# Kernel tuning notes

Measured on AMD Instinct MI355X. Metric: run time of the kernel, lower is better.

Reference implementation:

```python
import jax, jax.numpy as jnp
import numpy as np

B, T, C, H, E, K = 4, 2048, 1024, 2048, 8, 2


def setup_inputs() -> dict:
    key = jax.random.key(0)
    ks = jax.random.split(key, 9)
    s = lambda k, shape, fan: jax.random.normal(k, shape, jnp.float32) / np.sqrt(fan)
    return {
        "x": jax.random.normal(ks[0], (B, T, C), jnp.float32),
        "gate_w": s(ks[1], (C, E), C),            # router gate (no bias)
        "sg_w": s(ks[2], (C, H), C),              # shared expert: gate proj
        "su_w": s(ks[3], (C, H), C),              # shared expert: up proj
        "sd_w": s(ks[4], (H, C), H),              # shared expert: down proj
        "eg_w": s(ks[5], (E, C, H), C),           # routed experts: gate proj
        "eu_w": s(ks[6], (E, C, H), C),           # routed experts: up proj
        "ed_w": s(ks[7], (E, H, C), H),           # routed experts: down proj
    }


def _swiglu(x, wg, wu, wd):
    # x: (B,T,C) -> (B,T,C)
    return jnp.einsum("bth,hc->btc", jax.nn.silu(jnp.einsum("btc,ch->bth", x, wg)) * jnp.einsum("btc,ch->bth", x, wu), wd)


def reference(x, gate_w, sg_w, su_w, sd_w, eg_w, eu_w, ed_w):
    # Router: top-k over expert logits, softmax over selected logits
    logits = jnp.einsum("btc,ce->bte", x, gate_w)            # (B,T,E)
    topk_logits, topk_idx = jax.lax.top_k(logits, K)         # (B,T,K)
    weights = jax.nn.softmax(topk_logits, axis=-1)           # (B,T,K)
    # Dense per-expert combine weight: w_e[b,t,e] = sum_k weights*(idx==e)
    onehot = jax.nn.one_hot(topk_idx, E, dtype=x.dtype)      # (B,T,K,E)
    dense_w = jnp.einsum("btk,btke->bte", weights, onehot)   # (B,T,E)

    shared_out = _swiglu(x, sg_w, su_w, sd_w)

    # Scan over experts (small fixed E), accumulating weighted expert outputs.
    dense_w_e = jnp.moveaxis(dense_w, -1, 0)                 # (E,B,T)

    def step(acc, params):
        wg, wu, wd, w = params
        return acc + w[..., None] * _swiglu(x, wg, wu, wd), None

    expert_out, _ = jax.lax.scan(step, jnp.zeros_like(x), (eg_w, eu_w, ed_w, dense_w_e))
    return shared_out + expert_out, logits
```

## Files before the change

### kernel.cpp

```cpp
#include <hip/hip_runtime.h>
#include <cstdint>
#include <cstddef>

#define NTOK 8192
#define CDIM 1024
#define HDIM 2048
#define NEXP 8
#define NSEG 9
#define MAXTILES 104

typedef __bf16 bf16;
typedef unsigned short u16;
typedef __attribute__((ext_vector_type(8))) __bf16 bf16x8;
typedef __attribute__((ext_vector_type(4))) float f32x4;

__device__ __forceinline__ u16 f2bf(float f) {
  union { u16 u; __bf16 b; } cv;
  cv.b = (__bf16)f;
  return cv.u;
}

__device__ __forceinline__ void gload_lds16(const bf16* g, bf16* l) {
  __builtin_amdgcn_global_load_lds(
      (const __attribute__((address_space(1))) unsigned int*)g,
      (__attribute__((address_space(3))) unsigned int*)l, 16, 0, 0);
}

__global__ __launch_bounds__(64) void init_kernel(int* __restrict__ counts,
                                                  int* __restrict__ fill) {
  if (threadIdx.x < NEXP) {
    counts[threadIdx.x] = 0;
    fill[threadIdx.x] = 0;
  }
}

__global__ __launch_bounds__(256) void zero_out_kernel(float* __restrict__ out) {
  size_t i = ((size_t)blockIdx.x * 256 + threadIdx.x) * 8;
  float4 z = {0.f, 0.f, 0.f, 0.f};
  *(float4*)(out + i) = z;
  *(float4*)(out + i + 4) = z;
}

__global__ __launch_bounds__(256) void cast_x_kernel(
    const float* __restrict__ src, bf16* __restrict__ dst) {
  size_t i = ((size_t)blockIdx.x * 256 + threadIdx.x) * 8;
  float4 a = *(const float4*)(src + i);
  float4 b = *(const float4*)(src + i + 4);
  bf16x8 p;
  p[0] = (bf16)a.x; p[1] = (bf16)a.y; p[2] = (bf16)a.z; p[3] = (bf16)a.w;
  p[4] = (bf16)b.x; p[5] = (bf16)b.y; p[6] = (bf16)b.z; p[7] = (bf16)b.w;
  *(bf16x8*)(dst + i) = p;
}

__global__ __launch_bounds__(256) void router2_kernel(
    const float* __restrict__ x, const float* __restrict__ gw,
    float* __restrict__ logits_out, int* __restrict__ tk_e,
    float* __restrict__ tk_w, int* __restrict__ counts) {
  int wv = threadIdx.x >> 6, l = threadIdx.x & 63;
  int t = blockIdx.x * 4 + wv;
  const float* xr = x + (size_t)t * CDIM;
  float acc[NEXP];
#pragma unroll
  for (int e = 0; e < NEXP; ++e) acc[e] = 0.f;
  for (int c = l; c < CDIM; c += 64) {
    float xv = xr[c];
    const float* g = gw + (size_t)c * NEXP;
    float4 g0 = *(const float4*)(g);
    float4 g1 = *(const float4*)(g + 4);
    acc[0] += xv * g0.x; acc[1] += xv * g0.y; acc[2] += xv * g0.z; acc[3] += xv * g0.w;
    acc[4] += xv * g1.x; acc[5] += xv * g1.y; acc[6] += xv * g1.z; acc[7] += xv * g1.w;
  }
#pragma unroll
  for (int off = 32; off > 0; off >>= 1) {
#pragma unroll
    for (int e = 0; e < NEXP; ++e) acc[e] += __shfl_xor(acc[e], off, 64);
  }
  int e0 = 0; float l0 = acc[0];
#pragma unroll
  for (int e = 1; e < NEXP; ++e) { if (acc[e] > l0) { l0 = acc[e]; e0 = e; } }
  int e1 = -1; float l1 = -3.4e38f;
#pragma unroll
  for (int e = 0; e < NEXP; ++e) { if (e != e0 && acc[e] > l1) { l1 = acc[e]; e1 = e; } }
  float ex = expf(l1 - l0);
  float w0 = 1.f / (1.f + ex), w1 = ex / (1.f + ex);
  if (l < NEXP) logits_out[(size_t)t * NEXP + l] = acc[l];
  if (l == 0) {
    tk_e[2 * t] = e0; tk_e[2 * t + 1] = e1;
    tk_w[2 * t] = w0; tk_w[2 * t + 1] = w1;
    atomicAdd(&counts[e0], 1);
    atomicAdd(&counts[e1], 1);
  }
}

__global__ __launch_bounds__(256) void offsets_kernel(
    const int* __restrict__ counts, int* __restrict__ offs_g,
    int* __restrict__ tile_seg, int* __restrict__ list_tok,
    float* __restrict__ w_row) {
  __shared__ int off[NSEG], pad[NSEG], cnt[NSEG], ntot;
  int tid = threadIdx.x;
  if (tid == 0) {
    int tot = 0;
    for (int e = 0; e < NSEG; ++e) {
      int c = (e < NEXP) ? counts[e] : NTOK;
      cnt[e] = c; off[e] = tot;
      int p = (c + 255) & ~255;
      pad[e] = p; tot += p;
    }
    ntot = tot;
  }
  __syncthreads();
  if (tid < NSEG) offs_g[tid] = off[tid];
  for (int gt = tid; gt < MAXTILES; gt += 256) {
    int row = gt * 256, seg = -1;
    if (row < ntot) {
      for (int e = 0; e < NSEG; ++e)
        if (row >= off[e] && row < off[e] + pad[e]) { seg = e; break; }
    }
    tile_seg[gt] = seg;
  }
  for (int e = 0; e < NSEG; ++e)
    for (int i = off[e] + cnt[e] + tid; i < off[e] + pad[e]; i += 256) {
      list_tok[i] = 0;
      w_row[i] = 0.f;
    }
}

__global__ __launch_bounds__(256) void scatter_kernel(
    const int* __restrict__ tk_e, const float* __restrict__ tk_w,
    const int* __restrict__ offs, int* __restrict__ fill,
    int* __restrict__ list_tok, float* __restrict__ w_row) {
  int t = blockIdx.x * 256 + threadIdx.x;
  int e0 = tk_e[2 * t], e1 = tk_e[2 * t + 1];
  float w0 = tk_w[2 * t], w1 = tk_w[2 * t + 1];
  int p0 = atomicAdd(&fill[e0], 1);
  int i0 = offs[e0] + p0;
  list_tok[i0] = t; w_row[i0] = w0;
  int p1 = atomicAdd(&fill[e1], 1);
  int i1 = offs[e1] + p1;
  list_tok[i1] = t; w_row[i1] = w1;
  int rsh = offs[NEXP] + t;
  list_tok[rsh] = t; w_row[rsh] = 1.f;
}

__device__ __forceinline__ void transpose_body(const float* __restrict__ src,
                                               u16* __restrict__ dst, int R, int C) {
  __shared__ u16 tile[64][65];
  int r0 = blockIdx.y * 64, c0 = blockIdx.x * 64;
  int tr = threadIdx.x >> 2;
  int tc = (threadIdx.x & 3) * 16;
  const float* s = src + (size_t)(r0 + tr) * C + c0 + tc;
  float4 f[4];
#pragma unroll
  for (int q = 0; q < 4; ++q) f[q] = *(const float4*)(s + q * 4);
#pragma unroll
  for (int q = 0; q < 4; ++q) {
    tile[tr][tc + q * 4 + 0] = f2bf(f[q].x);
    tile[tr][tc + q * 4 + 1] = f2bf(f[q].y);
    tile[tr][tc + q * 4 + 2] = f2bf(f[q].z);
    tile[tr][tc + q * 4 + 3] = f2bf(f[q].w);
  }
  __syncthreads();
  union { uint4 v[2]; u16 e[16]; } u;
#pragma unroll
  for (int j = 0; j < 16; ++j) u.e[j] = tile[tc + j][tr];
  u16* d = dst + (size_t)(c0 + tr) * R + r0 + tc;
  *(uint4*)d = u.v[0];
  *(uint4*)(d + 8) = u.v[1];
}

__global__ __launch_bounds__(256) void transpose_cast_kernel(
    const float* __restrict__ src, u16* __restrict__ dst, int R, int C) {
  transpose_body(src, dst, R, C);
}

__global__ __launch_bounds__(256) void transpose_gu_kernel(
    const float* __restrict__ sg, const float* __restrict__ su,
    const float* __restrict__ eg, const float* __restrict__ eu,
    u16* __restrict__ wTg, u16* __restrict__ wTu) {
  const size_t slot = (size_t)HDIM * CDIM;
  int z = blockIdx.z;
  const float* src; u16* dst;
  if (z == 0)       { src = sg;                 dst = wTg + 8 * slot; }
  else if (z == 1)  { src = su;                 dst = wTu + 8 * slot; }
  else if (z < 10)  { src = eg + (z - 2) * slot;  dst = wTg + (z - 2) * slot; }
  else              { src = eu + (z - 10) * slot; dst = wTu + (z - 10) * slot; }
  transpose_body(src, dst, CDIM, HDIM);
}

__global__ __launch_bounds__(256) void transpose_d_kernel(
    const float* __restrict__ sd, const float* __restrict__ ed,
    u16* __restrict__ wTd) {
  const size_t slot = (size_t)HDIM * CDIM;
  int z = blockIdx.z;
  const float* src; u16* dst;
  if (z == 0) { src = sd;                 dst = wTd + 8 * slot; }
  else        { src = ed + (z - 1) * slot; dst = wTd + (z - 1) * slot; }
  transpose_body(src, dst, HDIM, CDIM);
}


__global__ __launch_bounds__(512, 2) void gemm_gu2(
    const bf16* __restrict__ xb, const bf16* __restrict__ wTg,
    const bf16* __restrict__ wTu, const int* __restrict__ tile_seg,
    const int* __restrict__ list_tok, bf16* __restrict__ act) {
  __shared__ __align__(16) bf16 sA[2][256 * 64];
  __shared__ __align__(16) bf16 sBg[2][128 * 64];
  __shared__ __align__(16) bf16 sBu[2][128 * 64];
  __shared__ int tokLds[256];

  const int nwg = gridDim.x;
  const int bid = blockIdx.x;
  const int wid = (bid & 7) * (nwg >> 3) + (bid >> 3);
  const int tileIdx = wid % MAXTILES;
  const int colIdx = wid / MAXTILES;
  const int seg = tile_seg[tileIdx];
  if (seg < 0) return;

  const int tid = threadIdx.x, l = tid & 63, wv = tid >> 6;
  const int wr = wv >> 1, wc = wv & 1;
  const int n0 = colIdx * 128;
  const size_t rowbase = (size_t)tileIdx * 256;

  if (tid < 256) tokLds[tid] = list_tok[rowbase + tid];
  __syncthreads();

  const int srow = tid >> 3;
  const int scolSw = ((tid & 7) ^ (srow & 7)) << 3;
  const bf16* baseA[4];
#pragma unroll
  for (int q = 0; q < 4; ++q)
    baseA[q] = xb + (size_t)tokLds[q * 64 + srow] * CDIM + scolSw;
  const size_t wslot = (size_t)seg * HDIM * CDIM;
  const bf16* baseBg[2];
  const bf16* baseBu[2];
#pragma unroll
  for (int q = 0; q < 2; ++q) {
    const size_t r = (size_t)(n0 + q * 64 + srow) * CDIM + scolSw;
    baseBg[q] = wTg + wslot + r;
    baseBu[q] = wTu + wslot + r;
  }
  const int ldst = tid * 8;

  const int fr = l & 15;
  const int aRowB = (wr * 64 + fr) * 128;
  const int bRowB = (wc * 64 + fr) * 128;
  const int cSw0 = (((l >> 4) ^ (l & 7)) << 4);
  const int cSw1 = (((4 | (l >> 4)) ^ (l & 7)) << 4);

  f32x4 accG[4][4], accU[4][4];
#pragma unroll
  for (int i = 0; i < 4; ++i)
#pragma unroll
    for (int j = 0; j < 4; ++j) {
      accG[i][j] = (f32x4){0.f, 0.f, 0.f, 0.f};
      accU[i][j] = (f32x4){0.f, 0.f, 0.f, 0.f};
    }

  auto stage = [&](int b, int k0) {
#pragma unroll
    for (int q = 0; q < 4; ++q)
      gload_lds16(baseA[q] + k0, &sA[b][q * 4096 + ldst]);
#pragma unroll
    for (int q = 0; q < 2; ++q) {
      gload_lds16(baseBg[q] + k0, &sBg[b][q * 4096 + ldst]);
      gload_lds16(baseBu[q] + k0, &sBu[b][q * 4096 + ldst]);
    }
  };
  auto compute = [&](int b) {
    const char* pA = (const char*)&sA[b][0];
    const char* pG = (const char*)&sBg[b][0];
    const char* pU = (const char*)&sBu[b][0];
#pragma unroll
    for (int kk = 0; kk < 2; ++kk) {
      const int cSw = kk ? cSw1 : cSw0;
      bf16x8 af[4], bg[4], bu[4];
#pragma unroll
      for (int i = 0; i < 4; ++i) af[i] = *(const bf16x8*)(pA + aRowB + i * 2048 + cSw);
#pragma unroll
      for (int j = 0; j < 4; ++j) bg[j] = *(const bf16x8*)(pG + bRowB + j * 2048 + cSw);
#pragma unroll
      for (int j = 0; j < 4; ++j) bu[j] = *(const bf16x8*)(pU + bRowB + j * 2048 + cSw);
#pragma unroll
      for (int i = 0; i < 4; ++i)
#pragma unroll
        for (int j = 0; j < 4; ++j) {
          accG[i][j] = __builtin_amdgcn_mfma_f32_16x16x32_bf16(af[i], bg[j], accG[i][j], 0, 0, 0);
          accU[i][j] = __builtin_amdgcn_mfma_f32_16x16x32_bf16(af[i], bu[j], accU[i][j], 0, 0, 0);
        }
    }
  };

  const int NKT = CDIM / 64;
  stage(0, 0);
  for (int kt = 0; kt < NKT; kt += 2) {
    __syncthreads();
    stage(1, (kt + 1) * 64);
    compute(0);
    __syncthreads();
    if (kt + 2 < NKT) stage(0, (kt + 2) * 64);
    compute(1);
  }

  const int cn = n0 + wc * 64 + fr;
  const int rb = wr * 64 + (l >> 4) * 4;
#pragma unroll
  for (int i = 0; i < 4; ++i)
#pragma unroll
    for (int r = 0; r < 4; ++r) {
      const size_t row = rowbase + rb + i * 16 + r;
#pragma unroll
      for (int j = 0; j < 4; ++j) {
        float g = accG[i][j][r], u = accU[i][j][r];
        float s = g / (1.f + expf(-g));
        act[row * HDIM + cn + j * 16] = (bf16)(s * u);
      }
    }
}

__global__ __launch_bounds__(512, 2) void gemm_down2(
    const bf16* __restrict__ act, const bf16* __restrict__ wTd,
    const int* __restrict__ tile_seg, const int* __restrict__ list_tok,
    const float* __restrict__ w_row, float* __restrict__ out) {
  __shared__ __align__(16) bf16 sA[2][256 * 64];
  __shared__ __align__(16) bf16 sB[2][128 * 64];
  __shared__ int tokLds[256];
  __shared__ float wLds[256];

  const int nwg = gridDim.x;
  const int bid = blockIdx.x;
  const int wid = (bid & 7) * (nwg >> 3) + (bid >> 3);
  const int tileIdx = wid % MAXTILES;
  const int colIdx = wid / MAXTILES;
  const int seg = tile_seg[tileIdx];
  if (seg < 0) return;

  const int tid = threadIdx.x, l = tid & 63, wv = tid >> 6;
  const int wr = wv >> 1, wc = wv & 1;
  const int n0 = colIdx * 128;
  const size_t rowbase = (size_t)tileIdx * 256;

  if (tid < 256) tokLds[tid] = list_tok[rowbase + tid];
  else           wLds[tid - 256] = w_row[rowbase + tid - 256];
  __syncthreads();

  const int srow = tid >> 3;
  const int scolSw = ((tid & 7) ^ (srow & 7)) << 3;
  const bf16* baseA[4];
#pragma unroll
  for (int q = 0; q < 4; ++q)
    baseA[q] = act + (rowbase + q * 64 + srow) * HDIM + scolSw;
  const bf16* baseB[2];
#pragma unroll
  for (int q = 0; q < 2; ++q)
    baseB[q] = wTd + (size_t)seg * CDIM * HDIM + (size_t)(n0 + q * 64 + srow) * HDIM + scolSw;
  const int ldst = tid * 8;

  const int fr = l & 15;
  const int aRowB = (wr * 64 + fr) * 128;
  const int bRowB = (wc * 64 + fr) * 128;
  const int cSw0 = (((l >> 4) ^ (l & 7)) << 4);
  const int cSw1 = (((4 | (l >> 4)) ^ (l & 7)) << 4);

  f32x4 acc[4][4];
#pragma unroll
  for (int i = 0; i < 4; ++i)
#pragma unroll
    for (int j = 0; j < 4; ++j) acc[i][j] = (f32x4){0.f, 0.f, 0.f, 0.f};

  auto stage = [&](int b, int k0) {
#pragma unroll
    for (int q = 0; q < 4; ++q)
      gload_lds16(baseA[q] + k0, &sA[b][q * 4096 + ldst]);
#pragma unroll
    for (int q = 0; q < 2; ++q)
      gload_lds16(baseB[q] + k0, &sB[b][q * 4096 + ldst]);
  };
  auto compute = [&](int b) {
    const char* pA = (const char*)&sA[b][0];
    const char* pB = (const char*)&sB[b][0];
#pragma unroll
    for (int kk = 0; kk < 2; ++kk) {
      const int cSw = kk ? cSw1 : cSw0;
      bf16x8 af[4], bfr[4];
#pragma unroll
      for (int i = 0; i < 4; ++i) af[i] = *(const bf16x8*)(pA + aRowB + i * 2048 + cSw);
#pragma unroll
      for (int j = 0; j < 4; ++j) bfr[j] = *(const bf16x8*)(pB + bRowB + j * 2048 + cSw);
#pragma unroll
      for (int i = 0; i < 4; ++i)
#pragma unroll
        for (int j = 0; j < 4; ++j)
          acc[i][j] = __builtin_amdgcn_mfma_f32_16x16x32_bf16(af[i], bfr[j], acc[i][j], 0, 0, 0);
    }
  };

  const int NKT = HDIM / 64;
  stage(0, 0);
  for (int kt = 0; kt < NKT; kt += 2) {
    __syncthreads();
    stage(1, (kt + 1) * 64);
    compute(0);
    __syncthreads();
    if (kt + 2 < NKT) stage(0, (kt + 2) * 64);
    compute(1);
  }

  const int cn = n0 + wc * 64 + fr;
  const int rb = wr * 64 + (l >> 4) * 4;
#pragma unroll
  for (int i = 0; i < 4; ++i)
#pragma unroll
    for (int r = 0; r < 4; ++r) {
      const int lrow = rb + i * 16 + r;
      const float w = wLds[lrow];
      if (w != 0.f) {
        const int tok = tokLds[lrow];
        float* op = out + (size_t)tok * CDIM + cn;
#pragma unroll
        for (int j = 0; j < 4; ++j)
          atomicAdd(op + j * 16, w * acc[i][j][r]);
      }
    }
}

__global__ __launch_bounds__(256) void router_kernel(
    const float* __restrict__ x, const float* __restrict__ gw,
    float* __restrict__ dense_w, float* __restrict__ logits_out) {
  int wv = threadIdx.x >> 6, l = threadIdx.x & 63;
  int t = blockIdx.x * 4 + wv;
  const float* xr = x + (size_t)t * CDIM;
  float acc[NEXP];
#pragma unroll
  for (int e = 0; e < NEXP; ++e) acc[e] = 0.f;
  for (int c = l; c < CDIM; c += 64) {
    float xv = xr[c];
    const float* g = gw + (size_t)c * NEXP;
    float4 g0 = *(const float4*)(g);
    float4 g1 = *(const float4*)(g + 4);
    acc[0] += xv * g0.x; acc[1] += xv * g0.y; acc[2] += xv * g0.z; acc[3] += xv * g0.w;
    acc[4] += xv * g1.x; acc[5] += xv * g1.y; acc[6] += xv * g1.z; acc[7] += xv * g1.w;
  }
#pragma unroll
  for (int off = 32; off > 0; off >>= 1) {
#pragma unroll
    for (int e = 0; e < NEXP; ++e) acc[e] += __shfl_xor(acc[e], off, 64);
  }
  int e0 = 0; float l0 = acc[0];
#pragma unroll
  for (int e = 1; e < NEXP; ++e) { if (acc[e] > l0) { l0 = acc[e]; e0 = e; } }
  int e1 = -1; float l1 = -3.4e38f;
#pragma unroll
  for (int e = 0; e < NEXP; ++e) { if (e != e0 && acc[e] > l1) { l1 = acc[e]; e1 = e; } }
  float ex = expf(l1 - l0);
  float w0 = 1.f / (1.f + ex), w1 = ex / (1.f + ex);
  if (l < NEXP) {
    dense_w[(size_t)t * NEXP + l] = (l == e0) ? w0 : ((l == e1) ? w1 : 0.f);
    logits_out[(size_t)t * NEXP + l] = acc[l];
  }
}

template <int MODE>
__global__ __launch_bounds__(256) void gemm_bt(
    const bf16* __restrict__ A, const bf16* __restrict__ Bt,
    int K, int N,
    bf16* __restrict__ Dbf, const bf16* __restrict__ Gin,
    float* __restrict__ outAcc, const float* __restrict__ denseW, int expertId) {
  __shared__ __align__(16) bf16 sA[128 * 32];
  __shared__ __align__(16) bf16 sB[128 * 32];
  const int tid = threadIdx.x;
  const int l = tid & 63, wv = tid >> 6;
  const int wr = wv >> 1, wc = wv & 1;
  const int m0 = blockIdx.y * 128, n0 = blockIdx.x * 128;
  f32x4 acc[4][4];
#pragma unroll
  for (int i = 0; i < 4; ++i)
#pragma unroll
    for (int j = 0; j < 4; ++j) acc[i][j] = (f32x4){0.f, 0.f, 0.f, 0.f};
  const int srow = wv * 16 + (l >> 2);
  const int scol = (l & 3) * 8;
  const bf16* gA = A + (size_t)(m0 + srow) * K + scol;
  const bf16* gB = Bt + (size_t)(n0 + srow) * K + scol;
  bf16* lA = sA + srow * 32 + scol;
  bf16* lB = sB + srow * 32 + scol;
  const int fr = l & 15, fk = (l >> 4) * 8;
  const bf16* rA = sA + (size_t)(wr * 64 + fr) * 32 + fk;
  const bf16* rB = sB + (size_t)(wc * 64 + fr) * 32 + fk;
  for (int k0 = 0; k0 < K; k0 += 32) {
    __syncthreads();
    gload_lds16(gA, lA);
    gload_lds16(gA + (size_t)64 * K, lA + 64 * 32);
    gload_lds16(gB, lB);
    gload_lds16(gB + (size_t)64 * K, lB + 64 * 32);
    gA += 32; gB += 32;
    __syncthreads();
    bf16x8 af[4], bfr[4];
#pragma unroll
    for (int i = 0; i < 4; ++i) af[i] = *(const bf16x8*)(rA + i * 16 * 32);
#pragma unroll
    for (int j = 0; j < 4; ++j) bfr[j] = *(const bf16x8*)(rB + j * 16 * 32);
#pragma unroll
    for (int i = 0; i < 4; ++i)
#pragma unroll
      for (int j = 0; j < 4; ++j)
        acc[i][j] = __builtin_amdgcn_mfma_f32_16x16x32_bf16(af[i], bfr[j], acc[i][j], 0, 0, 0);
  }
  const int cn = n0 + wc * 64 + (l & 15);
  const int rb = m0 + wr * 64 + (l >> 4) * 4;
#pragma unroll
  for (int i = 0; i < 4; ++i)
#pragma unroll
    for (int r = 0; r < 4; ++r) {
      const int m = rb + i * 16 + r;
#pragma unroll
      for (int j = 0; j < 4; ++j) {
        const int n = cn + j * 16;
        float v = acc[i][j][r];
        if (MODE == 0) {
          Dbf[(size_t)m * N + n] = (bf16)v;
        } else if (MODE == 1) {
          float g = (float)Gin[(size_t)m * N + n];
          float s = g / (1.f + expf(-g));
          Dbf[(size_t)m * N + n] = (bf16)(s * v);
        } else if (MODE == 2) {
          outAcc[(size_t)m * N + n] = v;
        } else {
          float w = denseW[(size_t)m * NEXP + expertId];
          outAcc[(size_t)m * N + n] += w * v;
        }
      }
    }
}

extern "C" void kernel_launch(void* const* d_in, const int* in_sizes, int n_in,
                              void* d_out, int out_size, void* d_ws, size_t ws_size,
                              hipStream_t stream) {
  const float* x    = (const float*)d_in[0];
  const float* gate = (const float*)d_in[1];
  const float* sg   = (const float*)d_in[2];
  const float* su   = (const float*)d_in[3];
  const float* sd   = (const float*)d_in[4];
  const float* eg   = (const float*)d_in[5];
  const float* eu   = (const float*)d_in[6];
  const float* ed   = (const float*)d_in[7];
  float* out    = (float*)d_out;
  float* logits = out + (size_t)NTOK * CDIM;

  const size_t MB = 1u << 20;
  const size_t full_need = 226 * MB;

  if (ws_size >= full_need) {
    char* ws = (char*)d_ws;
    bf16*  xb   = (bf16*)(ws);
    bf16*  wTg  = (bf16*)(ws + 16 * MB);
    bf16*  wTu  = (bf16*)(ws + 52 * MB);
    bf16*  act  = (bf16*)(ws + 88 * MB);
    bf16*  wTd  = (bf16*)(ws + 16 * MB);
    char*  sm   = ws + 224 * MB;
    int*   list_tok = (int*)(sm);
    int*   tk_e     = (int*)(sm + 256 * 1024);
    float* tk_w     = (float*)(sm + 320 * 1024);
    int*   tile_seg = (int*)(sm + 384 * 1024);
    int*   counts   = (int*)(sm + 388 * 1024);
    int*   fill     = (int*)(sm + 389 * 1024);
    int*   offs     = (int*)(sm + 390 * 1024);
    float* w_row    = (float*)(sm + 400 * 1024);

    init_kernel<<<1, 64, 0, stream>>>(counts, fill);
    zero_out_kernel<<<NTOK * CDIM / (256 * 8), 256, 0, stream>>>(out);
    cast_x_kernel<<<NTOK * CDIM / (256 * 8), 256, 0, stream>>>(x, xb);
    router2_kernel<<<NTOK / 4, 256, 0, stream>>>(x, gate, logits, tk_e, tk_w, counts);
    offsets_kernel<<<1, 256, 0, stream>>>(counts, offs, tile_seg, list_tok, w_row);
    scatter_kernel<<<NTOK / 256, 256, 0, stream>>>(tk_e, tk_w, offs, fill, list_tok, w_row);

    dim3 tgu(HDIM / 64, CDIM / 64, 18);
    transpose_gu_kernel<<<tgu, 256, 0, stream>>>(sg, su, eg, eu, (u16*)wTg, (u16*)wTu);

    gemm_gu2<<<(HDIM / 128) * MAXTILES, 512, 0, stream>>>(xb, wTg, wTu, tile_seg, list_tok, act);

    dim3 tdd(CDIM / 64, HDIM / 64, 9);
    transpose_d_kernel<<<tdd, 256, 0, stream>>>(sd, ed, (u16*)wTd);

    gemm_down2<<<(CDIM / 128) * MAXTILES, 512, 0, stream>>>(act, wTd, tile_seg, list_tok, w_row, out);
    return;
  }

  char* ws = (char*)d_ws;
  bf16*  xb   = (bf16*)(ws);
  bf16*  wTgf = (bf16*)(ws + 16 * MB);
  bf16*  wTuf = (bf16*)(ws + 20 * MB);
  bf16*  wTdf = (bf16*)(ws + 24 * MB);
  bf16*  gbuf = (bf16*)(ws + 28 * MB);
  float* dw   = (float*)(ws + 60 * MB);
  if (ws_size < 60 * MB + (size_t)NTOK * NEXP * sizeof(float)) return;

  cast_x_kernel<<<NTOK * CDIM / (256 * 8), 256, 0, stream>>>(x, xb);
  router_kernel<<<NTOK / 4, 256, 0, stream>>>(x, gate, dw, logits);

  dim3 tg1(HDIM / 64, CDIM / 64);
  dim3 tg2(CDIM / 64, HDIM / 64);
  dim3 g1(HDIM / 128, NTOK / 128);
  dim3 g2(CDIM / 128, NTOK / 128);

  transpose_cast_kernel<<<tg1, 256, 0, stream>>>(sg, (u16*)wTgf, CDIM, HDIM);
  transpose_cast_kernel<<<tg1, 256, 0, stream>>>(su, (u16*)wTuf, CDIM, HDIM);
  transpose_cast_kernel<<<tg2, 256, 0, stream>>>(sd, (u16*)wTdf, HDIM, CDIM);
  gemm_bt<0><<<g1, 256, 0, stream>>>(xb, wTgf, CDIM, HDIM, gbuf, nullptr, nullptr, nullptr, 0);
  gemm_bt<1><<<g1, 256, 0, stream>>>(xb, wTuf, CDIM, HDIM, gbuf, gbuf, nullptr, nullptr, 0);
  gemm_bt<2><<<g2, 256, 0, stream>>>(gbuf, wTdf, HDIM, CDIM, nullptr, nullptr, out, nullptr, 0);

  for (int e = 0; e < NEXP; ++e) {
    const float* egp = eg + (size_t)e * CDIM * HDIM;
    const float* eup = eu + (size_t)e * CDIM * HDIM;
    const float* edp = ed + (size_t)e * HDIM * CDIM;
    transpose_cast_kernel<<<tg1, 256, 0, stream>>>(egp, (u16*)wTgf, CDIM, HDIM);
    transpose_cast_kernel<<<tg1, 256, 0, stream>>>(eup, (u16*)wTuf, CDIM, HDIM);
    transpose_cast_kernel<<<tg2, 256, 0, stream>>>(edp, (u16*)wTdf, HDIM, CDIM);
    gemm_bt<0><<<g1, 256, 0, stream>>>(xb, wTgf, CDIM, HDIM, gbuf, nullptr, nullptr, nullptr, 0);
    gemm_bt<1><<<g1, 256, 0, stream>>>(xb, wTuf, CDIM, HDIM, gbuf, gbuf, nullptr, nullptr, 0);
    gemm_bt<3><<<g2, 256, 0, stream>>>(gbuf, wTdf, HDIM, CDIM, nullptr, nullptr, out, dw, e);
  }
}
```

Measured before the change: 1.058 ms.

## Deepen GEMM prefetch with explicit vmcnt waits, barriers, and MFMA priority

Both the gate/up and down GEMM main loops keep two K tiles in flight. Each step waits with a partial vmcnt so that only the current tile's global-to-LDS loads must have landed, instead of a full __syncthreads. The next stage into the same buffer is issued mid-tile, once both LDS fragment halves have been read into registers behind a barrier. MFMA blocks are wrapped in s_setprio to favour matrix issue. The aim is to overlap global loads with compute more deeply, at the cost of fragile hand-tuned waitcnt values that must match the exact number of loads per stage.

```diff
diff --git a/kernel.cpp b/kernel.cpp
--- a/kernel.cpp
+++ b/kernel.cpp
@@ -266,40 +266,61 @@
       gload_lds16(baseBu[q] + k0, &sBu[b][q * 4096 + ldst]);
     }
   };
-  auto compute = [&](int b) {
+
+  constexpr int NKT = CDIM / 64;
+
+  auto tile_step = [&](int b, int ktile, bool last) {
+    if (last) asm volatile("s_waitcnt vmcnt(0)" ::: "memory");
+    else      asm volatile("s_waitcnt vmcnt(8)" ::: "memory");
+    __builtin_amdgcn_s_barrier();
     const char* pA = (const char*)&sA[b][0];
     const char* pG = (const char*)&sBg[b][0];
     const char* pU = (const char*)&sBu[b][0];
-#pragma unroll
-    for (int kk = 0; kk < 2; ++kk) {
-      const int cSw = kk ? cSw1 : cSw0;
-      bf16x8 af[4], bg[4], bu[4];
-#pragma unroll
-      for (int i = 0; i < 4; ++i) af[i] = *(const bf16x8*)(pA + aRowB + i * 2048 + cSw);
-#pragma unroll
-      for (int j = 0; j < 4; ++j) bg[j] = *(const bf16x8*)(pG + bRowB + j * 2048 + cSw);
-#pragma unroll
-      for (int j = 0; j < 4; ++j) bu[j] = *(const bf16x8*)(pU + bRowB + j * 2048 + cSw);
-#pragma unroll
-      for (int i = 0; i < 4; ++i)
-#pragma unroll
-        for (int j = 0; j < 4; ++j) {
-          accG[i][j] = __builtin_amdgcn_mfma_f32_16x16x32_bf16(af[i], bg[j], accG[i][j], 0, 0, 0);
-          accU[i][j] = __builtin_amdgcn_mfma_f32_16x16x32_bf16(af[i], bu[j], accU[i][j], 0, 0, 0);
-        }
-    }
+    bf16x8 af0[4], bg0[4], bu0[4];
+#pragma unroll
+    for (int i = 0; i < 4; ++i) af0[i] = *(const bf16x8*)(pA + aRowB + i * 2048 + cSw0);
+#pragma unroll
+    for (int j = 0; j < 4; ++j) bg0[j] = *(const bf16x8*)(pG + bRowB + j * 2048 + cSw0);
+#pragma unroll
+    for (int j = 0; j < 4; ++j) bu0[j] = *(const bf16x8*)(pU + bRowB + j * 2048 + cSw0);
+    __builtin_amdgcn_s_setprio(1);
+#pragma unroll
+    for (int i = 0; i < 4; ++i)
+#pragma unroll
+      for (int j = 0; j < 4; ++j) {
+        accG[i][j] = __builtin_amdgcn_mfma_f32_16x16x32_bf16(af0[i], bg0[j], accG[i][j], 0, 0, 0);
+        accU[i][j] = __builtin_amdgcn_mfma_f32_16x16x32_bf16(af0[i], bu0[j], accU[i][j], 0, 0, 0);
+      }
+    __builtin_amdgcn_s_setprio(0);
+    bf16x8 af1[4], bg1[4], bu1[4];
+#pragma unroll
+    for (int i = 0; i < 4; ++i) af1[i] = *(const bf16x8*)(pA + aRowB + i * 2048 + cSw1);
+#pragma unroll
+    for (int j = 0; j < 4; ++j) bg1[j] = *(const bf16x8*)(pG + bRowB + j * 2048 + cSw1);
+#pragma unroll
+    for (int j = 0; j < 4; ++j) bu1[j] = *(const bf16x8*)(pU + bRowB + j * 2048 + cSw1);
+    asm volatile("s_waitcnt lgkmcnt(0)" ::: "memory");
+    __builtin_amdgcn_s_barrier();
+    if (ktile + 2 < NKT) stage(b, (ktile + 2) * 64);
+    __builtin_amdgcn_s_setprio(1);
+#pragma unroll
+    for (int i = 0; i < 4; ++i)
+#pragma unroll
+      for (int j = 0; j < 4; ++j) {
+        accG[i][j] = __builtin_amdgcn_mfma_f32_16x16x32_bf16(af1[i], bg1[j], accG[i][j], 0, 0, 0);
+        accU[i][j] = __builtin_amdgcn_mfma_f32_16x16x32_bf16(af1[i], bu1[j], accU[i][j], 0, 0, 0);
+      }
+    __builtin_amdgcn_s_setprio(0);
   };
 
-  const int NKT = CDIM / 64;
   stage(0, 0);
-  for (int kt = 0; kt < NKT; kt += 2) {
-    __syncthreads();
-    stage(1, (kt + 1) * 64);
-    compute(0);
-    __syncthreads();
-    if (kt + 2 < NKT) stage(0, (kt + 2) * 64);
-    compute(1);
-  }
+  stage(1, 64);
+  for (int kt = 0; kt + 2 < NKT; kt += 2) {
+    tile_step(0, kt, false);
+    tile_step(1, kt + 1, false);
+  }
+  tile_step(0, NKT - 2, false);
+  tile_step(1, NKT - 1, true);
 
   const int cn = n0 + wc * 64 + fr;
   const int rb = wr * 64 + (l >> 4) * 4;
@@ -375,35 +396,52 @@
     for (int q = 0; q < 2; ++q)
       gload_lds16(baseB[q] + k0, &sB[b][q * 4096 + ldst]);
   };
-  auto compute = [&](int b) {
+
+  constexpr int NKT = HDIM / 64;
+
+  auto tile_step = [&](int b, int ktile, bool last) {
+    if (last) asm volatile("s_waitcnt vmcnt(0)" ::: "memory");
+    else      asm volatile("s_waitcnt vmcnt(6)" ::: "memory");
+    __builtin_amdgcn_s_barrier();
     const char* pA = (const char*)&sA[b][0];
     const char* pB = (const char*)&sB[b][0];
-#pragma unroll
-    for (int kk = 0; kk < 2; ++kk) {
-      const int cSw = kk ? cSw1 : cSw0;
-      bf16x8 af[4], bfr[4];
-#pragma unroll
-      for (int i = 0; i < 4; ++i) af[i] = *(const bf16x8*)(pA + aRowB + i * 2048 + cSw);
-#pragma unroll
-      for (int j = 0; j < 4; ++j) bfr[j] = *(const bf16x8*)(pB + bRowB + j * 2048 + cSw);
-#pragma unroll
-      for (int i = 0; i < 4; ++i)
-#pragma unroll
-        for (int j = 0; j < 4; ++j)
-          acc[i][j] = __builtin_amdgcn_mfma_f32_16x16x32_bf16(af[i], bfr[j], acc[i][j], 0, 0, 0);
-    }
+    bf16x8 af0[4], bf0[4];
+#pragma unroll
+    for (int i = 0; i < 4; ++i) af0[i] = *(const bf16x8*)(pA + aRowB + i * 2048 + cSw0);
+#pragma unroll
+    for (int j = 0; j < 4; ++j) bf0[j] = *(const bf16x8*)(pB + bRowB + j * 2048 + cSw0);
+    __builtin_amdgcn_s_setprio(1);
+#pragma unroll
+    for (int i = 0; i < 4; ++i)
+#pragma unroll
+      for (int j = 0; j < 4; ++j)
+        acc[i][j] = __builtin_amdgcn_mfma_f32_16x16x32_bf16(af0[i], bf0[j], acc[i][j], 0, 0, 0);
+    __builtin_amdgcn_s_setprio(0);
+    bf16x8 af1[4], bf1[4];
+#pragma unroll
+    for (int i = 0; i < 4; ++i) af1[i] = *(const bf16x8*)(pA + aRowB + i * 2048 + cSw1);
+#pragma unroll
+    for (int j = 0; j < 4; ++j) bf1[j] = *(const bf16x8*)(pB + bRowB + j * 2048 + cSw1);
+    asm volatile("s_waitcnt lgkmcnt(0)" ::: "memory");
+    __builtin_amdgcn_s_barrier();
+    if (ktile + 2 < NKT) stage(b, (ktile + 2) * 64);
+    __builtin_amdgcn_s_setprio(1);
+#pragma unroll
+    for (int i = 0; i < 4; ++i)
+#pragma unroll
+      for (int j = 0; j < 4; ++j)
+        acc[i][j] = __builtin_amdgcn_mfma_f32_16x16x32_bf16(af1[i], bf1[j], acc[i][j], 0, 0, 0);
+    __builtin_amdgcn_s_setprio(0);
   };
 
-  const int NKT = HDIM / 64;
   stage(0, 0);
-  for (int kt = 0; kt < NKT; kt += 2) {
-    __syncthreads();
-    stage(1, (kt + 1) * 64);
-    compute(0);
-    __syncthreads();
-    if (kt + 2 < NKT) stage(0, (kt + 2) * 64);
-    compute(1);
-  }
+  stage(1, 64);
+  for (int kt = 0; kt + 2 < NKT; kt += 2) {
+    tile_step(0, kt, false);
+    tile_step(1, kt + 1, false);
+  }
+  tile_step(0, NKT - 2, false);
+  tile_step(1, NKT - 1, true);
 
   const int cn = n0 + wc * 64 + fr;
   const int rb = wr * 64 + (l >> 4) * 4;
```

New measurement: 971.5 us. -8.1%, faster.

## Rework MoE GEMMs with BK=32 double-buffered pipeline, smaller LDS, higher occupancy

Applied to the files above, without the earlier changes.

Both the grouped gate/up GEMM and the down GEMM are rewritten with a K-step of 32 and a single packed LDS buffer per stage. Loads are issued two stages ahead with explicit vmcnt waits and raw barriers, and s_setprio is raised around the MFMA block. The gate/up kernel moves to 128-row tiles (twice as many tiles) with 8 waves laid out 2x4. Launch bounds go to 4 blocks per CU to raise occupancy and overlap memory with compute, at the cost of more barriers per K and smaller per-wave tiles.

```diff
diff --git a/kernel.cpp b/kernel.cpp
--- a/kernel.cpp
+++ b/kernel.cpp
@@ -8,6 +8,7 @@
 #define NEXP 8
 #define NSEG 9
 #define MAXTILES 104
+#define GUTILES (MAXTILES * 2)
 
 typedef __bf16 bf16;
 typedef unsigned short u16;
@@ -199,14 +200,111 @@
 }
 
 
-__global__ __launch_bounds__(512, 2) void gemm_gu2(
+__global__ __launch_bounds__(512, 4) void gemm_gu3(
     const bf16* __restrict__ xb, const bf16* __restrict__ wTg,
     const bf16* __restrict__ wTu, const int* __restrict__ tile_seg,
     const int* __restrict__ list_tok, bf16* __restrict__ act) {
-  __shared__ __align__(16) bf16 sA[2][256 * 64];
-  __shared__ __align__(16) bf16 sBg[2][128 * 64];
-  __shared__ __align__(16) bf16 sBu[2][128 * 64];
+  __shared__ __align__(16) bf16 sS[2][12288];
+  __shared__ int tokLds[128];
+
+  const int nwg = gridDim.x;
+  const int bid = blockIdx.x;
+  const int wid = (bid & 7) * (nwg >> 3) + (bid >> 3);
+  const int tileIdx = wid % GUTILES;
+  const int colIdx = wid / GUTILES;
+  const int seg = tile_seg[tileIdx >> 1];
+  if (seg < 0) return;
+
+  const int tid = threadIdx.x, l = tid & 63, wv = tid >> 6;
+  const int wr = wv >> 2, wn = wv & 3;
+  const int n0 = colIdx * 128;
+  const size_t rowbase = (size_t)tileIdx * 128;
+
+  if (tid < 128) tokLds[tid] = list_tok[rowbase + tid];
+  __syncthreads();
+
+  const int srow = 2 * (tid >> 3) + ((tid >> 2) & 1);
+  const int scol = (((tid & 3) ^ ((tid >> 3) & 3)) << 3);
+  const bf16* gA = xb + (size_t)tokLds[srow] * CDIM + scol;
+  const size_t wslot = (size_t)seg * HDIM * CDIM;
+  const bf16* gBg = wTg + wslot + (size_t)(n0 + srow) * CDIM + scol;
+  const bf16* gBu = wTu + wslot + (size_t)(n0 + srow) * CDIM + scol;
+  const int ldst = tid * 8;
+
+  const int fr = l & 15, u = l >> 4;
+  const int laneRd = (fr >> 1) * 128 + (fr & 1) * 64 + ((u ^ ((fr >> 1) & 3)) << 4);
+  const int aOff = (wr * 64) * 64 + laneRd;
+  const int bOff = (wn * 32) * 64 + laneRd;
+
+  f32x4 accG[4][2], accU[4][2];
+#pragma unroll
+  for (int i = 0; i < 4; ++i)
+#pragma unroll
+    for (int j = 0; j < 2; ++j) {
+      accG[i][j] = (f32x4){0.f, 0.f, 0.f, 0.f};
+      accU[i][j] = (f32x4){0.f, 0.f, 0.f, 0.f};
+    }
+
+  auto stage = [&](int b, int k0) {
+    bf16* d = &sS[b][0] + ldst;
+    gload_lds16(gA + k0, d);
+    gload_lds16(gBg + k0, d + 4096);
+    gload_lds16(gBu + k0, d + 8192);
+  };
+
+  constexpr int NKT = CDIM / 32;
+  stage(0, 0);
+  stage(1, 32);
+  for (int kt = 0; kt < NKT; ++kt) {
+    if (kt < NKT - 1) asm volatile("s_waitcnt vmcnt(3)" ::: "memory");
+    else              asm volatile("s_waitcnt vmcnt(0)" ::: "memory");
+    __builtin_amdgcn_s_barrier();
+    const char* pS = (const char*)&sS[kt & 1][0];
+    bf16x8 af[4], bg[2], bu[2];
+#pragma unroll
+    for (int i = 0; i < 4; ++i) af[i] = *(const bf16x8*)(pS + aOff + i * 1024);
+#pragma unroll
+    for (int j = 0; j < 2; ++j) {
+      bg[j] = *(const bf16x8*)(pS + 8192 + bOff + j * 1024);
+      bu[j] = *(const bf16x8*)(pS + 16384 + bOff + j * 1024);
+    }
+    asm volatile("s_waitcnt lgkmcnt(0)" ::: "memory");
+    __builtin_amdgcn_s_barrier();
+    if (kt + 2 < NKT) stage(kt & 1, (kt + 2) * 32);
+    __builtin_amdgcn_s_setprio(1);
+#pragma unroll
+    for (int i = 0; i < 4; ++i)
+#pragma unroll
+      for (int j = 0; j < 2; ++j) {
+        accG[i][j] = __builtin_amdgcn_mfma_f32_16x16x32_bf16(af[i], bg[j], accG[i][j], 0, 0, 0);
+        accU[i][j] = __builtin_amdgcn_mfma_f32_16x16x32_bf16(af[i], bu[j], accU[i][j], 0, 0, 0);
+      }
+    __builtin_amdgcn_s_setprio(0);
+  }
+
+  const int cn = n0 + wn * 32 + fr;
+  const int rb = wr * 64 + (l >> 4) * 4;
+#pragma unroll
+  for (int i = 0; i < 4; ++i)
+#pragma unroll
+    for (int r = 0; r < 4; ++r) {
+      const size_t row = rowbase + rb + i * 16 + r;
+#pragma unroll
+      for (int j = 0; j < 2; ++j) {
+        float g = accG[i][j][r], uu = accU[i][j][r];
+        float s = g / (1.f + expf(-g));
+        act[row * HDIM + cn + j * 16] = (bf16)(s * uu);
+      }
+    }
+}
+
+__global__ __launch_bounds__(512, 4) void gemm_down3(
+    const bf16* __restrict__ act, const bf16* __restrict__ wTd,
+    const int* __restrict__ tile_seg, const int* __restrict__ list_tok,
+    const float* __restrict__ w_row, float* __restrict__ out) {
+  __shared__ __align__(16) bf16 sS[2][12288];
   __shared__ int tokLds[256];
+  __shared__ float wLds[256];
 
   const int nwg = gridDim.x;
   const int bid = blockIdx.x;
@@ -222,144 +320,20 @@
   const size_t rowbase = (size_t)tileIdx * 256;
 
   if (tid < 256) tokLds[tid] = list_tok[rowbase + tid];
-  __syncthreads();
-
-  const int srow = tid >> 3;
-  const int scolSw = ((tid & 7) ^ (srow & 7)) << 3;
-  const bf16* baseA[4];
-#pragma unroll
-  for (int q = 0; q < 4; ++q)
-    baseA[q] = xb + (size_t)tokLds[q * 64 + srow] * CDIM + scolSw;
-  const size_t wslot = (size_t)seg * HDIM * CDIM;
-  const bf16* baseBg[2];
-  const bf16* baseBu[2];
-#pragma unroll
-  for (int q = 0; q < 2; ++q) {
-    const size_t r = (size_t)(n0 + q * 64 + srow) * CDIM + scolSw;
-    baseBg[q] = wTg + wslot + r;
-    baseBu[q] = wTu + wslot + r;
-  }
-  const int ldst = tid * 8;
-
-  const int fr = l & 15;
-  const int aRowB = (wr * 64 + fr) * 128;
-  const int bRowB = (wc * 64 + fr) * 128;
-  const int cSw0 = (((l >> 4) ^ (l & 7)) << 4);
-  const int cSw1 = (((4 | (l >> 4)) ^ (l & 7)) << 4);
-
-  f32x4 accG[4][4], accU[4][4];
-#pragma unroll
-  for (int i = 0; i < 4; ++i)
-#pragma unroll
-    for (int j = 0; j < 4; ++j) {
-      accG[i][j] = (f32x4){0.f, 0.f, 0.f, 0.f};
-      accU[i][j] = (f32x4){0.f, 0.f, 0.f, 0.f};
-    }
-
-  auto stage = [&](int b, int k0) {
-#pragma unroll
-    for (int q = 0; q < 4; ++q)
-      gload_lds16(baseA[q] + k0, &sA[b][q * 4096 + ldst]);
-#pragma unroll
-    for (int q = 0; q < 2; ++q) {
-      gload_lds16(baseBg[q] + k0, &sBg[b][q * 4096 + ldst]);
-      gload_lds16(baseBu[q] + k0, &sBu[b][q * 4096 + ldst]);
-    }
-  };
-  auto compute = [&](int b) {
-    const char* pA = (const char*)&sA[b][0];
-    const char* pG = (const char*)&sBg[b][0];
-    const char* pU = (const char*)&sBu[b][0];
-#pragma unroll
-    for (int kk = 0; kk < 2; ++kk) {
-      const int cSw = kk ? cSw1 : cSw0;
-      bf16x8 af[4], bg[4], bu[4];
-#pragma unroll
-      for (int i = 0; i < 4; ++i) af[i] = *(const bf16x8*)(pA + aRowB + i * 2048 + cSw);
-#pragma unroll
-      for (int j = 0; j < 4; ++j) bg[j] = *(const bf16x8*)(pG + bRowB + j * 2048 + cSw);
-#pragma unroll
-      for (int j = 0; j < 4; ++j) bu[j] = *(const bf16x8*)(pU + bRowB + j * 2048 + cSw);
-#pragma unroll
-      for (int i = 0; i < 4; ++i)
-#pragma unroll
-        for (int j = 0; j < 4; ++j) {
-          accG[i][j] = __builtin_amdgcn_mfma_f32_16x16x32_bf16(af[i], bg[j], accG[i][j], 0, 0, 0);
-          accU[i][j] = __builtin_amdgcn_mfma_f32_16x16x32_bf16(af[i], bu[j], accU[i][j], 0, 0, 0);
-        }
-    }
-  };
-
-  const int NKT = CDIM / 64;
-  stage(0, 0);
-  for (int kt = 0; kt < NKT; kt += 2) {
-    __syncthreads();
-    stage(1, (kt + 1) * 64);
-    compute(0);
-    __syncthreads();
-    if (kt + 2 < NKT) stage(0, (kt + 2) * 64);
-    compute(1);
-  }
-
-  const int cn = n0 + wc * 64 + fr;
-  const int rb = wr * 64 + (l >> 4) * 4;
-#pragma unroll
-  for (int i = 0; i < 4; ++i)
-#pragma unroll
-    for (int r = 0; r < 4; ++r) {
-      const size_t row = rowbase + rb + i * 16 + r;
-#pragma unroll
-      for (int j = 0; j < 4; ++j) {
-        float g = accG[i][j][r], u = accU[i][j][r];
-        float s = g / (1.f + expf(-g));
-        act[row * HDIM + cn + j * 16] = (bf16)(s * u);
-      }
-    }
-}
-
-__global__ __launch_bounds__(512, 2) void gemm_down2(
-    const bf16* __restrict__ act, const bf16* __restrict__ wTd,
-    const int* __restrict__ tile_seg, const int* __restrict__ list_tok,
-    const float* __restrict__ w_row, float* __restrict__ out) {
-  __shared__ __align__(16) bf16 sA[2][256 * 64];
-  __shared__ __align__(16) bf16 sB[2][128 * 64];
-  __shared__ int tokLds[256];
-  __shared__ float wLds[256];
-
-  const int nwg = gridDim.x;
-  const int bid = blockIdx.x;
-  const int wid = (bid & 7) * (nwg >> 3) + (bid >> 3);
-  const int tileIdx = wid % MAXTILES;
-  const int colIdx = wid / MAXTILES;
-  const int seg = tile_seg[tileIdx];
-  if (seg < 0) return;
-
-  const int tid = threadIdx.x, l = tid & 63, wv = tid >> 6;
-  const int wr = wv >> 1, wc = wv & 1;
-  const int n0 = colIdx * 128;
-  const size_t rowbase = (size_t)tileIdx * 256;
-
-  if (tid < 256) tokLds[tid] = list_tok[rowbase + tid];
   else           wLds[tid - 256] = w_row[rowbase + tid - 256];
   __syncthreads();
 
-  const int srow = tid >> 3;
-  const int scolSw = ((tid & 7) ^ (srow & 7)) << 3;
-  const bf16* baseA[4];
-#pragma unroll
-  for (int q = 0; q < 4; ++q)
-    baseA[q] = act + (rowbase + q * 64 + srow) * HDIM + scolSw;
-  const bf16* baseB[2];
-#pragma unroll
-  for (int q = 0; q < 2; ++q)
-    baseB[q] = wTd + (size_t)seg * CDIM * HDIM + (size_t)(n0 + q * 64 + srow) * HDIM + scolSw;
+  const int srow = 2 * (tid >> 3) + ((tid >> 2) & 1);
+  const int scol = (((tid & 3) ^ ((tid >> 3) & 3)) << 3);
+  const bf16* gA0 = act + (rowbase + srow) * HDIM + scol;
+  const bf16* gA1 = act + (rowbase + 128 + srow) * HDIM + scol;
+  const bf16* gB  = wTd + (size_t)seg * CDIM * HDIM + (size_t)(n0 + srow) * HDIM + scol;
   const int ldst = tid * 8;
 
-  const int fr = l & 15;
-  const int aRowB = (wr * 64 + fr) * 128;
-  const int bRowB = (wc * 64 + fr) * 128;
-  const int cSw0 = (((l >> 4) ^ (l & 7)) << 4);
-  const int cSw1 = (((4 | (l >> 4)) ^ (l & 7)) << 4);
+  const int fr = l & 15, u = l >> 4;
+  const int laneRd = (fr >> 1) * 128 + (fr & 1) * 64 + ((u ^ ((fr >> 1) & 3)) << 4);
+  const int aOff = (wr * 64) * 64 + laneRd;
+  const int bOff = 16384 + (wc * 64) * 64 + laneRd;
 
   f32x4 acc[4][4];
 #pragma unroll
@@ -368,41 +342,35 @@
     for (int j = 0; j < 4; ++j) acc[i][j] = (f32x4){0.f, 0.f, 0.f, 0.f};
 
   auto stage = [&](int b, int k0) {
-#pragma unroll
-    for (int q = 0; q < 4; ++q)
-      gload_lds16(baseA[q] + k0, &sA[b][q * 4096 + ldst]);
-#pragma unroll
-    for (int q = 0; q < 2; ++q)
-      gload_lds16(baseB[q] + k0, &sB[b][q * 4096 + ldst]);
+    bf16* d = &sS[b][0] + ldst;
+    gload_lds16(gA0 + k0, d);
+    gload_lds16(gA1 + k0, d + 4096);
+    gload_lds16(gB + k0, d + 8192);
   };
-  auto compute = [&](int b) {
-    const char* pA = (const char*)&sA[b][0];
-    const char* pB = (const char*)&sB[b][0];
-#pragma unroll
-    for (int kk = 0; kk < 2; ++kk) {
-      const int cSw = kk ? cSw1 : cSw0;
-      bf16x8 af[4], bfr[4];
-#pragma unroll
-      for (int i = 0; i < 4; ++i) af[i] = *(const bf16x8*)(pA + aRowB + i * 2048 + cSw);
-#pragma unroll
-      for (int j = 0; j < 4; ++j) bfr[j] = *(const bf16x8*)(pB + bRowB + j * 2048 + cSw);
-#pragma unroll
-      for (int i = 0; i < 4; ++i)
-#pragma unroll
-        for (int j = 0; j < 4; ++j)
-          acc[i][j] = __builtin_amdgcn_mfma_f32_16x16x32_bf16(af[i], bfr[j], acc[i][j], 0, 0, 0);
-    }
-  };
-
-  const int NKT = HDIM / 64;
+
+  constexpr int NKT = HDIM / 32;
   stage(0, 0);
-  for (int kt = 0; kt < NKT; kt += 2) {
-    __syncthreads();
-    stage(1, (kt + 1) * 64);
-    compute(0);
-    __syncthreads();
-    if (kt + 2 < NKT) stage(0, (kt + 2) * 64);
-    compute(1);
+  stage(1, 32);
+  for (int kt = 0; kt < NKT; ++kt) {
+    if (kt < NKT - 1) asm volatile("s_waitcnt vmcnt(3)" ::: "memory");
+    else              asm volatile("s_waitcnt vmcnt(0)" ::: "memory");
+    __builtin_amdgcn_s_barrier();
+    const char* pS = (const char*)&sS[kt & 1][0];
+    bf16x8 af[4], bf[4];
+#pragma unroll
+    for (int i = 0; i < 4; ++i) af[i] = *(const bf16x8*)(pS + aOff + i * 1024);
+#pragma unroll
+    for (int j = 0; j < 4; ++j) bf[j] = *(const bf16x8*)(pS + bOff + j * 1024);
+    asm volatile("s_waitcnt lgkmcnt(0)" ::: "memory");
+    __builtin_amdgcn_s_barrier();
+    if (kt + 2 < NKT) stage(kt & 1, (kt + 2) * 32);
+    __builtin_amdgcn_s_setprio(1);
+#pragma unroll
+    for (int i = 0; i < 4; ++i)
+#pragma unroll
+      for (int j = 0; j < 4; ++j)
+        acc[i][j] = __builtin_amdgcn_mfma_f32_16x16x32_bf16(af[i], bf[j], acc[i][j], 0, 0, 0);
+    __builtin_amdgcn_s_setprio(0);
   }
 
   const int cn = n0 + wc * 64 + fr;
@@ -575,12 +543,12 @@
     dim3 tgu(HDIM / 64, CDIM / 64, 18);
     transpose_gu_kernel<<<tgu, 256, 0, stream>>>(sg, su, eg, eu, (u16*)wTg, (u16*)wTu);
 
-    gemm_gu2<<<(HDIM / 128) * MAXTILES, 512, 0, stream>>>(xb, wTg, wTu, tile_seg, list_tok, act);
+    gemm_gu3<<<(HDIM / 128) * GUTILES, 512, 0, stream>>>(xb, wTg, wTu, tile_seg, list_tok, act);
 
     dim3 tdd(CDIM / 64, HDIM / 64, 9);
     transpose_d_kernel<<<tdd, 256, 0, stream>>>(sd, ed, (u16*)wTd);
 
-    gemm_down2<<<(CDIM / 128) * MAXTILES, 512, 0, stream>>>(act, wTd, tile_seg, list_tok, w_row, out);
+    gemm_down3<<<(CDIM / 128) * MAXTILES, 512, 0, stream>>>(act, wTd, tile_seg, list_tok, w_row, out);
     return;
   }
 
```

Measured after the change: 970.6 us. -8.2%, faster.
